# Performance work log

Hardware: AMD Instinct MI355X
Metric: run time of the kernel (lower is better)

## Reference

```python
import jax, jax.numpy as jnp
import numpy as np

B, C_IN, C_OUT, K, L = 8, 512, 512, 5, 4096
RED = 128  # max(int(512*0.25), 4)
STRIDE, PAD, DIL, GROUPS = 1, 2, 1, 1


def setup_inputs() -> dict:
    key = jax.random.key(0)
    ks = jax.random.split(key, 20)

    def n(k, shape, scale=0.05):
        return jax.random.normal(k, shape, jnp.float32) * scale

    inp = {
        "x": jax.random.normal(ks[0], (B, C_IN, L), jnp.float32),
        "weight": n(ks[1], (C_OUT, C_IN // GROUPS, K), 0.05),
        "bias": jnp.zeros((C_OUT,), jnp.float32),
    }
    # four attention branches: avgpool -> 1x1 conv (C_in->RED) -> relu -> 1x1 conv (RED->out) -> sigmoid
    for i, (nm, od) in enumerate(zip(["ka", "sa", "ia", "oa"], [K, 1, C_IN, C_OUT])):
        inp[nm + "_w1"] = n(ks[2 + 4 * i], (RED, C_IN))
        inp[nm + "_b1"] = jnp.zeros((RED,), jnp.float32)
        inp[nm + "_w2"] = n(ks[3 + 4 * i], (od, RED))
        inp[nm + "_b2"] = jnp.zeros((od,), jnp.float32)
    return inp


def _att(avg, w1, b1, w2, b2):
    # avg: [B, C_in]; two 1x1 convs over a length-1 signal == two dense layers
    h = jax.nn.relu(avg @ w1.T + b1)
    return jax.nn.sigmoid(h @ w2.T + b2)


def reference(x, weight, bias,
              ka_w1, ka_b1, ka_w2, ka_b2,
              sa_w1, sa_b1, sa_w2, sa_b2,
              ia_w1, ia_b1, ia_w2, ia_b2,
              oa_w1, oa_b1, oa_w2, oa_b2):
    b, c, l = x.shape
    avg = x.mean(axis=2)                     # AdaptiveAvgPool1d(1) -> [B, C_in]
    ka = _att(avg, ka_w1, ka_b1, ka_w2, ka_b2)  # [B, K]
    sa = _att(avg, sa_w1, sa_b1, sa_w2, sa_b2)  # [B, 1]
    ia = _att(avg, ia_w1, ia_b1, ia_w2, ia_b2)  # [B, C_in]
    oa = _att(avg, oa_w1, oa_b1, oa_w2, oa_b2)  # [B, C_out]
    # dynamic weight [B, C_out, C_in//g, K]; note ia broadcasts on the OUT-channel
    # axis (faithful to the torch broadcasting, which requires C_in == C_out)
    dw = (weight[None]
          * ka[:, None, None, :]
          * sa[:, :, None, None]
          * ia[:, :, None, None]
          * oa[:, :, None, None])
    dw = dw.reshape(b * C_OUT, C_IN // GROUPS, K)
    xg = x.reshape(1, b * c, l)
    out = jax.lax.conv_general_dilated(
        xg, dw,
        window_strides=(STRIDE,),
        padding=[(PAD, PAD)],
        rhs_dilation=(DIL,),
        feature_group_count=b * GROUPS,
        dimension_numbers=("NCH", "OIH", "NCH"))
    out = out.reshape(b, C_OUT, -1) + bias[None, :, None]
    return out
```

## Files before the change

kernel.cpp:

```cpp
#include <hip/hip_runtime.h>

typedef unsigned short u16;
typedef __bf16 bf16x8 __attribute__((ext_vector_type(8)));
typedef float f32x4 __attribute__((ext_vector_type(4)));
typedef u16 u16x8 __attribute__((ext_vector_type(8)));

#define B_    8
#define CIN   512
#define COUT  512
#define KT    5
#define LEN   4096
#define RED_  128
#define KDIM  (KT * CIN)
#define XTROWS (LEN + 4)
#define NLT   (LEN / 32)

__device__ __forceinline__ u16 f2bf(float f) {
    unsigned int u = __float_as_uint(f);
    u += 0x7fffu + ((u >> 16) & 1u);
    return (u16)(u >> 16);
}

typedef __attribute__((address_space(1))) void gvoid_t;
typedef __attribute__((address_space(3))) void lvoid_t;
__device__ __forceinline__ void glds16(const u16* g, u16* l) {
    __builtin_amdgcn_global_load_lds((gvoid_t*)g, (lvoid_t*)l, 16, 0, 0);
}

#define TPAD 72
__global__ void xtavg_kernel(const float* __restrict__ x, u16* __restrict__ xt,
                             float* __restrict__ P) {
    __shared__ __align__(16) u16 T[32 * TPAD];
    const int b  = blockIdx.z;
    const int l0 = blockIdx.x * 32;
    const int c0 = blockIdx.y * 64;
    const int tid = threadIdx.x;
    const int lw = tid & 31;
    const int cg = tid >> 5;
    const int l  = l0 + lw;
    const int c8 = c0 + cg * 8;

    const float* xp = x + ((size_t)b * CIN + c8) * LEN + l;
    float f[8];
#pragma unroll
    for (int j = 0; j < 8; ++j) f[j] = xp[(size_t)j * LEN];

    unsigned d[4];
#pragma unroll
    for (int j = 0; j < 4; ++j)
        d[j] = __builtin_amdgcn_perm(__float_as_uint(f[2 * j + 1]),
                                     __float_as_uint(f[2 * j]), 0x07060302);
    *(uint4*)&T[lw * TPAD + cg * 8] = make_uint4(d[0], d[1], d[2], d[3]);

#pragma unroll
    for (int j = 0; j < 8; ++j) {
        float s = f[j];
#pragma unroll
        for (int off = 16; off > 0; off >>= 1) s += __shfl_down(s, off, 32);
        if (lw == 0) P[(size_t)blockIdx.x * (B_ * CIN) + b * CIN + c8 + j] = s;
    }
    __syncthreads();

    const int r = tid >> 3, cc = (tid & 7) * 8;
    *(uint4*)(xt + ((size_t)b * XTROWS + l0 + 2 + r) * CIN + c0 + cc) =
        *(const uint4*)&T[r * TPAD + cc];

    if (blockIdx.y == 0 && l0 == 0 && tid < 128)
        *(uint4*)(xt + ((size_t)b * XTROWS + (tid >> 6)) * CIN + (tid & 63) * 8) =
            make_uint4(0, 0, 0, 0);
    if (blockIdx.y == 0 && l0 == LEN - 32 && tid < 128)
        *(uint4*)(xt + ((size_t)b * XTROWS + LEN + 2 + (tid >> 6)) * CIN + (tid & 63) * 8) =
            make_uint4(0, 0, 0, 0);
}

__global__ void attn_kernel(const float* __restrict__ P,
    const float* kw1, const float* kb1, const float* kw2, const float* kb2,
    const float* sw1, const float* sb1, const float* sw2, const float* sb2,
    const float* iw1, const float* ib1, const float* iw2, const float* ib2,
    const float* ow1, const float* ob1, const float* ow2, const float* ob2,
    float* __restrict__ ka, float* __restrict__ sa,
    float* __restrict__ ia, float* __restrict__ oa) {
    const int br = blockIdx.x >> 3, b = blockIdx.x & 7;
    const float *w1, *b1p, *w2, *b2p; float* op; int od;
    if (br == 0)      { w1 = kw1; b1p = kb1; w2 = kw2; b2p = kb2; op = ka + b * KT;  od = KT;   }
    else if (br == 1) { w1 = sw1; b1p = sb1; w2 = sw2; b2p = sb2; op = sa + b;       od = 1;    }
    else if (br == 2) { w1 = iw1; b1p = ib1; w2 = iw2; b2p = ib2; op = ia + b * CIN; od = CIN;  }
    else              { w1 = ow1; b1p = ob1; w2 = ow2; b2p = ob2; op = oa + b * COUT; od = COUT; }

    __shared__ float av[4 * 132];
    __shared__ float h[RED_];
    const int t = threadIdx.x;
    {
        const float* pp = P + b * CIN + t;
        float ssum = 0.f;
#pragma unroll 8
        for (int lt = 0; lt < NLT; ++lt) ssum += pp[(size_t)lt * (B_ * CIN)];
        av[(t >> 7) * 132 + (t & 127)] = ssum * (1.0f / LEN);
    }
    __syncthreads();

    const int row = t >> 2, part = t & 3;
    float acc = 0.f;
    const float4* wr = (const float4*)(w1 + (size_t)row * CIN + part * 128);
    const float* ap = &av[part * 132];
#pragma unroll 8
    for (int c = 0; c < 32; ++c) {
        float4 w = wr[c];
        acc += ap[4 * c] * w.x + ap[4 * c + 1] * w.y + ap[4 * c + 2] * w.z + ap[4 * c + 3] * w.w;
    }
    acc += __shfl_down(acc, 1, 64);
    acc += __shfl_down(acc, 2, 64);
    if (part == 0) h[row] = fmaxf(acc + b1p[row], 0.f);
    __syncthreads();

    for (int o = t; o < od; o += 512) {
        float a2 = b2p[o];
        const float4* w2r = (const float4*)(w2 + (size_t)o * RED_);
#pragma unroll 8
        for (int j = 0; j < RED_ / 4; ++j) {
            float4 w = w2r[j];
            a2 += h[4 * j] * w.x + h[4 * j + 1] * w.y + h[4 * j + 2] * w.z + h[4 * j + 3] * w.w;
        }
        op[o] = 1.f / (1.f + expf(-a2));
    }
}

__global__ void wbgen_kernel(const float* __restrict__ w, const float* __restrict__ ka,
                             u16* __restrict__ wb) {
    __shared__ float kv[B_ * KT];
    const int tid = threadIdx.x;
    if (tid < B_ * KT) kv[tid] = ka[tid];
    __syncthreads();
    const int o  = (blockIdx.x >> 2) * 4 + (tid >> 6);
    const int b0 = (blockIdx.x & 3) * 2;
    const int i8 = (tid & 63) * 8;

    const float* wp = w + ((size_t)o * CIN + i8) * KT;
    float wv[40];
#pragma unroll
    for (int q = 0; q < 10; ++q) {
        float4 v = ((const float4*)wp)[q];
        wv[4 * q] = v.x; wv[4 * q + 1] = v.y; wv[4 * q + 2] = v.z; wv[4 * q + 3] = v.w;
    }
#pragma unroll
    for (int bb = 0; bb < 2; ++bb) {
        const int b = b0 + bb;
#pragma unroll
        for (int k = 0; k < KT; ++k) {
            const float s = kv[b * KT + k];
            u16x8 r;
#pragma unroll
            for (int j = 0; j < 8; ++j) r[j] = f2bf(wv[j * KT + k] * s);
            *(u16x8*)(wb + ((size_t)(b * COUT + o)) * KDIM + k * CIN + i8) = r;
        }
    }
}

__global__ __launch_bounds__(256, 2) void gemm_kernel(
    const u16* __restrict__ wb, const u16* __restrict__ xt,
    const float* __restrict__ sa, const float* __restrict__ ia,
    const float* __restrict__ oa, const float* __restrict__ bias,
    float* __restrict__ out) {
    __shared__ __align__(16) u16 As[5 * 128 * 32];
    __shared__ __align__(16) u16 Bs[260 * 32];
    __shared__ float sm[128], bm[128];

    const int orig = blockIdx.x;
    const int wg   = (orig & 7) * 64 + (orig >> 3);
    const int l0 = (wg & 15) * 256;
    const int o0 = ((wg >> 4) & 3) * 128;
    const int b  = wg >> 6;
    const int tid = threadIdx.x;

    if (tid < 128) {
        sm[tid] = sa[b] * ia[b * CIN + o0 + tid] * oa[b * COUT + o0 + tid];
        bm[tid] = bias[o0 + tid];
    }

    const int lane = tid & 63;
    const int wave = tid >> 6;
    const int wm = (wave >> 1) * 64;
    const int wn = (wave & 1) * 128;
    const int lm = lane & 15;
    const int quad = lane >> 4;

    f32x4 acc[4][8];
#pragma unroll
    for (int i = 0; i < 4; ++i)
#pragma unroll
        for (int j = 0; j < 8; ++j) {
            f32x4 zz = {0.f, 0.f, 0.f, 0.f};
            acc[i][j] = zz;
        }

    const u16* gA = wb + ((size_t)(b * COUT + o0 + (tid >> 2))) * KDIM + (tid & 3) * 8;
    const u16* gB = xt + ((size_t)b * XTROWS + l0) * CIN;

#pragma unroll 1
    for (int ic = 0; ic < 16; ++ic) {
        const int i0 = ic * 32;
#pragma unroll
        for (int t = 0; t < KT; ++t) {
            glds16(gA + t * 512 + i0, &As[t * 4096 + tid * 8]);
            glds16(gA + (size_t)64 * KDIM + t * 512 + i0, &As[t * 4096 + 2048 + tid * 8]);
        }
#pragma unroll
        for (int r = 0; r < 4; ++r) {
            const int slot = r * 256 + tid;
            glds16(gB + (size_t)(slot >> 2) * CIN + i0 + (slot & 3) * 8, &Bs[slot * 8]);
        }
        if (tid < 16)
            glds16(gB + (size_t)(256 + (tid >> 2)) * CIN + i0 + (tid & 3) * 8,
                   &Bs[(1024 + tid) * 8]);
        __syncthreads();

#pragma unroll
        for (int t = 0; t < KT; ++t) {
            bf16x8 af[4], bfr[8];
#pragma unroll
            for (int f = 0; f < 4; ++f)
                af[f] = *(const bf16x8*)&As[t * 4096 + (wm + f * 16 + lm) * 32 + quad * 8];
#pragma unroll
            for (int f = 0; f < 8; ++f)
                bfr[f] = *(const bf16x8*)&Bs[(wn + f * 16 + lm + t) * 32 + quad * 8];
#pragma unroll
            for (int mt = 0; mt < 4; ++mt)
#pragma unroll
                for (int nt = 0; nt < 8; ++nt)
                    acc[mt][nt] = __builtin_amdgcn_mfma_f32_16x16x32_bf16(
                        af[mt], bfr[nt], acc[mt][nt], 0, 0, 0);
        }
        __syncthreads();
    }

#pragma unroll
    for (int mt = 0; mt < 4; ++mt) {
        const int mb = wm + mt * 16 + quad * 4;
        float sv[4], bv[4];
#pragma unroll
        for (int r = 0; r < 4; ++r) { sv[r] = sm[mb + r]; bv[r] = bm[mb + r]; }
#pragma unroll
        for (int nt = 0; nt < 8; ++nt) {
            const int col = l0 + wn + nt * 16 + lm;
            float* op = out + ((size_t)(b * COUT + o0 + mb)) * LEN + col;
#pragma unroll
            for (int r = 0; r < 4; ++r)
                op[(size_t)r * LEN] = sv[r] * acc[mt][nt][r] + bv[r];
        }
    }
}

extern "C" void kernel_launch(void* const* d_in, const int* in_sizes, int n_in,
                              void* d_out, int out_size, void* d_ws, size_t ws_size,
                              hipStream_t stream) {
    const float* x      = (const float*)d_in[0];
    const float* weight = (const float*)d_in[1];
    const float* bias   = (const float*)d_in[2];
    float* out = (float*)d_out;

    char* ws = (char*)d_ws;
    size_t off = 0;
    auto alloc = [&](size_t bytes) {
        void* p = ws + off;
        off += (bytes + 255) & ~(size_t)255;
        return p;
    };
    u16*   wbuf = (u16*)alloc((size_t)B_ * COUT * KDIM * sizeof(u16));
    u16*   xtb  = (u16*)alloc((size_t)B_ * XTROWS * CIN * sizeof(u16));
    float* Pbuf = (float*)alloc((size_t)NLT * B_ * CIN * sizeof(float));
    float* ka   = (float*)alloc((size_t)B_ * KT * sizeof(float));
    float* sa   = (float*)alloc((size_t)B_ * sizeof(float));
    float* ia   = (float*)alloc((size_t)B_ * CIN * sizeof(float));
    float* oa   = (float*)alloc((size_t)B_ * COUT * sizeof(float));

    xtavg_kernel<<<dim3(LEN / 32, CIN / 64, B_), 256, 0, stream>>>(x, xtb, Pbuf);
    attn_kernel<<<32, 512, 0, stream>>>(Pbuf,
        (const float*)d_in[3],  (const float*)d_in[4],  (const float*)d_in[5],  (const float*)d_in[6],
        (const float*)d_in[7],  (const float*)d_in[8],  (const float*)d_in[9],  (const float*)d_in[10],
        (const float*)d_in[11], (const float*)d_in[12], (const float*)d_in[13], (const float*)d_in[14],
        (const float*)d_in[15], (const float*)d_in[16], (const float*)d_in[17], (const float*)d_in[18],
        ka, sa, ia, oa);
    wbgen_kernel<<<(COUT / 4) * 4, 256, 0, stream>>>(weight, ka, wbuf);
    gemm_kernel<<<512, 256, 0, stream>>>(
        wbuf, xtb, sa, ia, oa, bias, out);
}
```

Baseline: 246.4 us.

## Fuse attention and weight-generation kernels, recomputing kernel attention per block

Merges the attention kernel and the bf16 dynamic-weight generation kernel into one launch. The first 256 blocks each recompute the kernel-size attention branch for 4 batches, then scale and convert their slice of the weight. The remaining 24 blocks compute the spatial, input and output attention branches. This removes one launch and the serialization between the two kernels, at the cost of redundant attention recomputation and extra reads of the partial sums in every weight block.

New measurement: 301.9 us. +22.5%, slower.

```diff
diff --git a/kernel.cpp b/kernel.cpp
--- a/kernel.cpp
+++ b/kernel.cpp
@@ -14,6 +14,7 @@
 #define KDIM  (KT * CIN)
 #define XTROWS (LEN + 4)
 #define NLT   (LEN / 32)
+#define TPAD  72
 
 __device__ __forceinline__ u16 f2bf(float f) {
     unsigned int u = __float_as_uint(f);
@@ -27,7 +28,6 @@
     __builtin_amdgcn_global_load_lds((gvoid_t*)g, (lvoid_t*)l, 16, 0, 0);
 }
 
-#define TPAD 72
 __global__ void xtavg_kernel(const float* __restrict__ x, u16* __restrict__ xt,
                              float* __restrict__ P) {
     __shared__ __align__(16) u16 T[32 * TPAD];
@@ -73,48 +73,34 @@
             make_uint4(0, 0, 0, 0);
 }
 
-__global__ void attn_kernel(const float* __restrict__ P,
-    const float* kw1, const float* kb1, const float* kw2, const float* kb2,
-    const float* sw1, const float* sb1, const float* sw2, const float* sb2,
-    const float* iw1, const float* ib1, const float* iw2, const float* ib2,
-    const float* ow1, const float* ob1, const float* ow2, const float* ob2,
-    float* __restrict__ ka, float* __restrict__ sa,
-    float* __restrict__ ia, float* __restrict__ oa) {
-    const int br = blockIdx.x >> 3, b = blockIdx.x & 7;
-    const float *w1, *b1p, *w2, *b2p; float* op; int od;
-    if (br == 0)      { w1 = kw1; b1p = kb1; w2 = kw2; b2p = kb2; op = ka + b * KT;  od = KT;   }
-    else if (br == 1) { w1 = sw1; b1p = sb1; w2 = sw2; b2p = sb2; op = sa + b;       od = 1;    }
-    else if (br == 2) { w1 = iw1; b1p = ib1; w2 = iw2; b2p = ib2; op = ia + b * CIN; od = CIN;  }
-    else              { w1 = ow1; b1p = ob1; w2 = ow2; b2p = ob2; op = oa + b * COUT; od = COUT; }
-
-    __shared__ float av[4 * 132];
-    __shared__ float h[RED_];
-    const int t = threadIdx.x;
-    {
-        const float* pp = P + b * CIN + t;
-        float ssum = 0.f;
+__device__ __forceinline__ void attn_branch(
+    int tid, const float* __restrict__ P,
+    const float* w1, const float* b1, const float* w2, const float* b2,
+    float* op, int od, int b, float* av, float* h) {
+#pragma unroll
+    for (int half = 0; half < 2; ++half) {
+        const int ch = tid + half * 256;
+        const float* pp = P + b * CIN + ch;
+        float s = 0.f;
 #pragma unroll 8
-        for (int lt = 0; lt < NLT; ++lt) ssum += pp[(size_t)lt * (B_ * CIN)];
-        av[(t >> 7) * 132 + (t & 127)] = ssum * (1.0f / LEN);
+        for (int lt = 0; lt < NLT; ++lt) s += pp[(size_t)lt * (B_ * CIN)];
+        av[ch] = s * (1.0f / LEN);
     }
     __syncthreads();
-
-    const int row = t >> 2, part = t & 3;
+    const int row = tid >> 1, part = tid & 1;
     float acc = 0.f;
-    const float4* wr = (const float4*)(w1 + (size_t)row * CIN + part * 128);
-    const float* ap = &av[part * 132];
+    const float4* wr = (const float4*)(w1 + (size_t)row * CIN + part * 256);
+    const float* ap = av + part * 256;
 #pragma unroll 8
-    for (int c = 0; c < 32; ++c) {
+    for (int c = 0; c < 64; ++c) {
         float4 w = wr[c];
         acc += ap[4 * c] * w.x + ap[4 * c + 1] * w.y + ap[4 * c + 2] * w.z + ap[4 * c + 3] * w.w;
     }
     acc += __shfl_down(acc, 1, 64);
-    acc += __shfl_down(acc, 2, 64);
-    if (part == 0) h[row] = fmaxf(acc + b1p[row], 0.f);
+    if (part == 0) h[row] = fmaxf(acc + b1[row], 0.f);
     __syncthreads();
-
-    for (int o = t; o < od; o += 512) {
-        float a2 = b2p[o];
+    for (int o = tid; o < od; o += 256) {
+        float a2 = b2[o];
         const float4* w2r = (const float4*)(w2 + (size_t)o * RED_);
 #pragma unroll 8
         for (int j = 0; j < RED_ / 4; ++j) {
@@ -125,34 +111,56 @@
     }
 }
 
-__global__ void wbgen_kernel(const float* __restrict__ w, const float* __restrict__ ka,
-                             u16* __restrict__ wb) {
-    __shared__ float kv[B_ * KT];
+__global__ void fusedprep_kernel(
+    const float* __restrict__ P, const float* __restrict__ weight,
+    const float* kw1, const float* kb1, const float* kw2, const float* kb2,
+    const float* sw1, const float* sb1, const float* sw2, const float* sb2,
+    const float* iw1, const float* ib1, const float* iw2, const float* ib2,
+    const float* ow1, const float* ob1, const float* ow2, const float* ob2,
+    float* __restrict__ sa, float* __restrict__ ia, float* __restrict__ oa,
+    u16* __restrict__ wb) {
+    __shared__ float av[CIN];
+    __shared__ float h[RED_];
+    __shared__ float kv[4 * KT];
     const int tid = threadIdx.x;
-    if (tid < B_ * KT) kv[tid] = ka[tid];
-    __syncthreads();
-    const int o  = (blockIdx.x >> 2) * 4 + (tid >> 6);
-    const int b0 = (blockIdx.x & 3) * 2;
-    const int i8 = (tid & 63) * 8;
-
-    const float* wp = w + ((size_t)o * CIN + i8) * KT;
-    float wv[40];
-#pragma unroll
-    for (int q = 0; q < 10; ++q) {
-        float4 v = ((const float4*)wp)[q];
-        wv[4 * q] = v.x; wv[4 * q + 1] = v.y; wv[4 * q + 2] = v.z; wv[4 * q + 3] = v.w;
-    }
-#pragma unroll
-    for (int bb = 0; bb < 2; ++bb) {
-        const int b = b0 + bb;
-#pragma unroll
-        for (int k = 0; k < KT; ++k) {
-            const float s = kv[b * KT + k];
-            u16x8 r;
-#pragma unroll
-            for (int j = 0; j < 8; ++j) r[j] = f2bf(wv[j * KT + k] * s);
-            *(u16x8*)(wb + ((size_t)(b * COUT + o)) * KDIM + k * CIN + i8) = r;
-        }
+
+    if (blockIdx.x < 256) {
+        const int og = (int)blockIdx.x >> 1;
+        const int b0 = ((int)blockIdx.x & 1) * 4;
+#pragma unroll 1
+        for (int bb = 0; bb < 4; ++bb) {
+            attn_branch(tid, P, kw1, kb1, kw2, kb2, &kv[bb * KT], KT, b0 + bb, av, h);
+            __syncthreads();
+        }
+        const int o  = og * 4 + (tid >> 6);
+        const int i8 = (tid & 63) * 8;
+        const float* wp = weight + ((size_t)o * CIN + i8) * KT;
+        float wv[40];
+#pragma unroll
+        for (int q = 0; q < 10; ++q) {
+            float4 v = ((const float4*)wp)[q];
+            wv[4 * q] = v.x; wv[4 * q + 1] = v.y; wv[4 * q + 2] = v.z; wv[4 * q + 3] = v.w;
+        }
+#pragma unroll
+        for (int bb = 0; bb < 4; ++bb) {
+            const int b = b0 + bb;
+#pragma unroll
+            for (int k = 0; k < KT; ++k) {
+                const float s = kv[bb * KT + k];
+                u16x8 r;
+#pragma unroll
+                for (int j = 0; j < 8; ++j) r[j] = f2bf(wv[j * KT + k] * s);
+                *(u16x8*)(wb + ((size_t)(b * COUT + o)) * KDIM + k * CIN + i8) = r;
+            }
+        }
+    } else {
+        const int vb = (int)blockIdx.x - 256;
+        const int br = vb >> 3, b = vb & 7;
+        const float *w1, *b1, *w2, *b2; float* op; int od;
+        if (br == 0)      { w1 = sw1; b1 = sb1; w2 = sw2; b2 = sb2; op = sa + b;        od = 1;    }
+        else if (br == 1) { w1 = iw1; b1 = ib1; w2 = iw2; b2 = ib2; op = ia + b * CIN;  od = CIN;  }
+        else              { w1 = ow1; b1 = ob1; w2 = ow2; b2 = ob2; op = oa + b * COUT; od = COUT; }
+        attn_branch(tid, P, w1, b1, w2, b2, op, od, b, av, h);
     }
 }
 
@@ -268,19 +276,16 @@
     u16*   wbuf = (u16*)alloc((size_t)B_ * COUT * KDIM * sizeof(u16));
     u16*   xtb  = (u16*)alloc((size_t)B_ * XTROWS * CIN * sizeof(u16));
     float* Pbuf = (float*)alloc((size_t)NLT * B_ * CIN * sizeof(float));
-    float* ka   = (float*)alloc((size_t)B_ * KT * sizeof(float));
     float* sa   = (float*)alloc((size_t)B_ * sizeof(float));
     float* ia   = (float*)alloc((size_t)B_ * CIN * sizeof(float));
     float* oa   = (float*)alloc((size_t)B_ * COUT * sizeof(float));
 
     xtavg_kernel<<<dim3(LEN / 32, CIN / 64, B_), 256, 0, stream>>>(x, xtb, Pbuf);
-    attn_kernel<<<32, 512, 0, stream>>>(Pbuf,
+    fusedprep_kernel<<<280, 256, 0, stream>>>(Pbuf, weight,
         (const float*)d_in[3],  (const float*)d_in[4],  (const float*)d_in[5],  (const float*)d_in[6],
         (const float*)d_in[7],  (const float*)d_in[8],  (const float*)d_in[9],  (const float*)d_in[10],
         (const float*)d_in[11], (const float*)d_in[12], (const float*)d_in[13], (const float*)d_in[14],
         (const float*)d_in[15], (const float*)d_in[16], (const float*)d_in[17], (const float*)d_in[18],
-        ka, sa, ia, oa);
-    wbgen_kernel<<<(COUT / 4) * 4, 256, 0, stream>>>(weight, ka, wbuf);
-    gemm_kernel<<<512, 256, 0, stream>>>(
-        wbuf, xtb, sa, ia, oa, bias, out);
-}
+        sa, ia, oa, wbuf);
+    gemm_kernel<<<512, 256, 0, stream>>>(wbuf, xtb, sa, ia, oa, bias, out);
+}
```

## Rewrite transpose/avg-pool kernel with float4 loads, larger tiles, LDS partial sums

Applied to the files above, without the earlier changes.

The transpose-to-bf16 and mean-pooling kernel now processes 64x128 tiles using float4 global loads, packs channel pairs into 32-bit LDS words, and replaces the per-channel shuffle reductions with LDS partial sums reduced by one thread per channel. The partial-sum buffer shrinks from 128 to 64 length tiles, which reduces the work the attention kernel does when reading it. The aim is wider, better-coalesced memory access and fewer shuffle instructions. In exchange the kernel uses more LDS per block and launches a smaller grid.

After: 241.2 us. 1.02x faster.

```diff
diff --git a/kernel.cpp b/kernel.cpp
--- a/kernel.cpp
+++ b/kernel.cpp
@@ -13,7 +13,7 @@
 #define RED_  128
 #define KDIM  (KT * CIN)
 #define XTROWS (LEN + 4)
-#define NLT   (LEN / 32)
+#define NLT   64
 
 __device__ __forceinline__ u16 f2bf(float f) {
     unsigned int u = __float_as_uint(f);
@@ -27,48 +27,60 @@
     __builtin_amdgcn_global_load_lds((gvoid_t*)g, (lvoid_t*)l, 16, 0, 0);
 }
 
-#define TPAD 72
-__global__ void xtavg_kernel(const float* __restrict__ x, u16* __restrict__ xt,
-                             float* __restrict__ P) {
-    __shared__ __align__(16) u16 T[32 * TPAD];
+__global__ __launch_bounds__(256) void xtavg_kernel(const float* __restrict__ x,
+                                                    u16* __restrict__ xt,
+                                                    float* __restrict__ P) {
+    __shared__ __align__(16) unsigned Tu[64 * 65];
+    __shared__ float Fp[64 * 2 * 17];
     const int b  = blockIdx.z;
-    const int l0 = blockIdx.x * 32;
-    const int c0 = blockIdx.y * 64;
+    const int l0 = blockIdx.x * 64;
+    const int c0 = blockIdx.y * 128;
     const int tid = threadIdx.x;
-    const int lw = tid & 31;
-    const int cg = tid >> 5;
-    const int l  = l0 + lw;
-    const int c8 = c0 + cg * 8;
-
-    const float* xp = x + ((size_t)b * CIN + c8) * LEN + l;
-    float f[8];
-#pragma unroll
-    for (int j = 0; j < 8; ++j) f[j] = xp[(size_t)j * LEN];
-
-    unsigned d[4];
-#pragma unroll
-    for (int j = 0; j < 4; ++j)
-        d[j] = __builtin_amdgcn_perm(__float_as_uint(f[2 * j + 1]),
-                                     __float_as_uint(f[2 * j]), 0x07060302);
-    *(uint4*)&T[lw * TPAD + cg * 8] = make_uint4(d[0], d[1], d[2], d[3]);
-
-#pragma unroll
-    for (int j = 0; j < 8; ++j) {
-        float s = f[j];
-#pragma unroll
-        for (int off = 16; off > 0; off >>= 1) s += __shfl_down(s, off, 32);
-        if (lw == 0) P[(size_t)blockIdx.x * (B_ * CIN) + b * CIN + c8 + j] = s;
-    }
-    __syncthreads();
-
-    const int r = tid >> 3, cc = (tid & 7) * 8;
-    *(uint4*)(xt + ((size_t)b * XTROWS + l0 + 2 + r) * CIN + c0 + cc) =
-        *(const uint4*)&T[r * TPAD + cc];
-
-    if (blockIdx.y == 0 && l0 == 0 && tid < 128)
+    const int lq  = tid & 15;
+    const int cpg = tid >> 4;
+
+#pragma unroll
+    for (int p = 0; p < 4; ++p) {
+        const int cp = p * 16 + cpg;
+        const int c  = c0 + cp * 2;
+        const float* xa = x + ((size_t)b * CIN + c) * LEN + l0 + lq * 4;
+        float4 va = *(const float4*)xa;
+        float4 vb = *(const float4*)(xa + LEN);
+        unsigned u0 = __builtin_amdgcn_perm(__float_as_uint(vb.x), __float_as_uint(va.x), 0x07060302);
+        unsigned u1 = __builtin_amdgcn_perm(__float_as_uint(vb.y), __float_as_uint(va.y), 0x07060302);
+        unsigned u2 = __builtin_amdgcn_perm(__float_as_uint(vb.z), __float_as_uint(va.z), 0x07060302);
+        unsigned u3 = __builtin_amdgcn_perm(__float_as_uint(vb.w), __float_as_uint(va.w), 0x07060302);
+        Tu[(lq * 4 + 0) * 65 + cp] = u0;
+        Tu[(lq * 4 + 1) * 65 + cp] = u1;
+        Tu[(lq * 4 + 2) * 65 + cp] = u2;
+        Tu[(lq * 4 + 3) * 65 + cp] = u3;
+        Fp[(cp * 2 + 0) * 17 + lq] = va.x + va.y + va.z + va.w;
+        Fp[(cp * 2 + 1) * 17 + lq] = vb.x + vb.y + vb.z + vb.w;
+    }
+    __syncthreads();
+
+#pragma unroll
+    for (int p = 0; p < 4; ++p) {
+        const int r  = p * 16 + (tid >> 4);
+        const int j4 = (tid & 15) * 4;
+        unsigned w0 = Tu[r * 65 + j4 + 0];
+        unsigned w1 = Tu[r * 65 + j4 + 1];
+        unsigned w2 = Tu[r * 65 + j4 + 2];
+        unsigned w3 = Tu[r * 65 + j4 + 3];
+        *(uint4*)(xt + ((size_t)b * XTROWS + l0 + 2 + r) * CIN + c0 + j4 * 2) =
+            make_uint4(w0, w1, w2, w3);
+    }
+    if (tid < 128) {
+        const float* fp = &Fp[tid * 17];
+        float s = 0.f;
+#pragma unroll
+        for (int k = 0; k < 16; ++k) s += fp[k];
+        P[(size_t)blockIdx.x * (B_ * CIN) + b * CIN + c0 + tid] = s;
+    }
+    if (blockIdx.y == 0 && blockIdx.x == 0 && tid < 128)
         *(uint4*)(xt + ((size_t)b * XTROWS + (tid >> 6)) * CIN + (tid & 63) * 8) =
             make_uint4(0, 0, 0, 0);
-    if (blockIdx.y == 0 && l0 == LEN - 32 && tid < 128)
+    if (blockIdx.y == 0 && blockIdx.x == (LEN / 64 - 1) && tid < 128)
         *(uint4*)(xt + ((size_t)b * XTROWS + LEN + 2 + (tid >> 6)) * CIN + (tid & 63) * 8) =
             make_uint4(0, 0, 0, 0);
 }
@@ -273,7 +285,7 @@
     float* ia   = (float*)alloc((size_t)B_ * CIN * sizeof(float));
     float* oa   = (float*)alloc((size_t)B_ * COUT * sizeof(float));
 
-    xtavg_kernel<<<dim3(LEN / 32, CIN / 64, B_), 256, 0, stream>>>(x, xtb, Pbuf);
+    xtavg_kernel<<<dim3(LEN / 64, CIN / 128, B_), 256, 0, stream>>>(x, xtb, Pbuf);
     attn_kernel<<<32, 512, 0, stream>>>(Pbuf,
         (const float*)d_in[3],  (const float*)d_in[4],  (const float*)d_in[5],  (const float*)d_in[6],
         (const float*)d_in[7],  (const float*)d_in[8],  (const float*)d_in[9],  (const float*)d_in[10],
@@ -281,6 +293,5 @@
         (const float*)d_in[15], (const float*)d_in[16], (const float*)d_in[17], (const float*)d_in[18],
         ka, sa, ia, oa);
     wbgen_kernel<<<(COUT / 4) * 4, 256, 0, stream>>>(weight, ka, wbuf);
-    gemm_kernel<<<512, 256, 0, stream>>>(
-        wbuf, xtb, sa, ia, oa, bias, out);
-}
+    gemm_kernel<<<512, 256, 0, stream>>>(wbuf, xtb, sa, ia, oa, bias, out);
+}
```
